# Kernel tuning notes

Measured on AMD Instinct MI355X. Metric: run time of the kernel, lower is better.

The kernel has to match this reference:

```python
import jax, jax.numpy as jnp
import numpy as np
from jax import lax

B, N, D_MODEL = 2, 1024, 512
D_INNER, D_STATE, D_CONV, DT_RANK, RED = 1024, 16, 4, 32, 4
EPS = 1e-5


def setup_inputs() -> dict:
    key = jax.random.key(0)
    ks = jax.random.split(key, 40)
    f32 = jnp.float32
    inp = {}
    inp["I1"] = jax.random.normal(ks[0], (B, N, D_MODEL), f32)
    inp["I2"] = jax.random.normal(ks[1], (B, N, D_MODEL), f32)
    inp["norm1_w"] = jnp.ones((D_MODEL,), f32)
    inp["norm1_b"] = jnp.zeros((D_MODEL,), f32)
    inp["norm2_w"] = jnp.ones((D_MODEL,), f32)
    inp["norm2_b"] = jnp.zeros((D_MODEL,), f32)
    inp["se_w1"] = jax.random.normal(ks[2], (D_MODEL // RED, D_MODEL), f32) * 0.02
    inp["se_w2"] = jax.random.normal(ks[3], (D_MODEL, D_MODEL // RED), f32) * 0.02
    A = jnp.tile(jnp.arange(1, D_STATE + 1, dtype=f32), (D_INNER, 1))  # (d_inner, d_state)
    for i, base in ((1, 4), (2, 14)):
        p = f"m{i}_"
        inp[p + "in_w"] = jax.random.normal(ks[base + 0], (2 * D_INNER, D_MODEL), f32) * 0.02
        inp[p + "conv_w"] = jax.random.normal(ks[base + 1], (D_INNER, 1, D_CONV), f32) * 0.1
        inp[p + "conv_b"] = jnp.zeros((D_INNER,), f32)
        inp[p + "xproj_w"] = jax.random.normal(ks[base + 2], (DT_RANK + 2 * D_STATE, D_INNER), f32) * 0.02
        inp[p + "dt_w"] = jax.random.normal(ks[base + 3], (D_INNER, DT_RANK), f32) * 0.02
        inp[p + "dt_b"] = jax.random.normal(ks[base + 4], (D_INNER,), f32) * 0.1
        inp[p + "A_log"] = jnp.log(A)
        inp[p + "D"] = jnp.ones((D_INNER,), f32)
        inp[p + "out_w"] = jax.random.normal(ks[base + 5], (D_MODEL, D_INNER), f32) * 0.02
    return inp


def layernorm(x, w, b):
    mu = x.mean(-1, keepdims=True)
    var = ((x - mu) ** 2).mean(-1, keepdims=True)
    return (x - mu) * lax.rsqrt(var + EPS) * w + b


def silu(x):
    return x * jax.nn.sigmoid(x)


def mamba(x, in_w, conv_w, conv_b, xproj_w, dt_w, dt_b, A_log, Dp, out_w):
    # x: (B, L, d_model)
    b, L, _ = x.shape
    xz = x @ in_w.T                        # (B, L, 2*d_inner)
    xc, z = jnp.split(xz, 2, axis=-1)
    # depthwise causal conv1d over L
    xc = xc.transpose(0, 2, 1)             # (B, d_inner, L)
    xc = jnp.pad(xc, ((0, 0), (0, 0), (D_CONV - 1, 0)))
    xc = lax.conv_general_dilated(xc, conv_w, (1,), "VALID",
                                  dimension_numbers=("NCH", "OIH", "NCH"),
                                  feature_group_count=D_INNER)
    xc = silu(xc + conv_b[None, :, None]).transpose(0, 2, 1)  # (B, L, d_inner)
    x_dbl = xc @ xproj_w.T                 # (B, L, dt_rank + 2*d_state)
    dt, Bm, Cm = jnp.split(x_dbl, [DT_RANK, DT_RANK + D_STATE], axis=-1)
    dt = jax.nn.softplus(dt @ dt_w.T + dt_b)      # (B, L, d_inner)
    A = -jnp.exp(A_log)                           # (d_inner, d_state)
    dA = jnp.exp(dt[..., None] * A)               # (B, L, d_inner, d_state)
    dBu = dt[..., None] * Bm[:, :, None, :] * xc[..., None]

    def step(h, inputs):
        dA_t, dBu_t, C_t = inputs
        h = dA_t * h + dBu_t                      # (B, d_inner, d_state)
        y = jnp.einsum("bds,bs->bd", h, C_t)
        return h, y

    h0 = jnp.zeros((b, D_INNER, D_STATE), x.dtype)
    _, ys = lax.scan(step, h0, (dA.transpose(1, 0, 2, 3),
                                dBu.transpose(1, 0, 2, 3),
                                Cm.transpose(1, 0, 2)))
    y = ys.transpose(1, 0, 2)                     # (B, L, d_inner)
    y = y + xc * Dp
    y = y * silu(z)
    return y @ out_w.T                            # (B, L, d_model)


def se_block(x, w1, w2):
    y = x.mean(axis=1)                            # (B, C)
    y = jax.nn.sigmoid(jax.nn.relu(y @ w1.T) @ w2.T)
    return x * y[:, None, :]


def channel_exchange(x1, x2):
    c = x1.shape[-1]
    mask = (jnp.arange(c) % 2 == 0)               # swap channels where c % p == 0
    return jnp.where(mask, x2, x1), jnp.where(mask, x1, x2)


def reference(I1, I2, norm1_w, norm1_b, norm2_w, norm2_b, se_w1, se_w2,
              m1_in_w, m1_conv_w, m1_conv_b, m1_xproj_w, m1_dt_w, m1_dt_b, m1_A_log, m1_D, m1_out_w,
              m2_in_w, m2_conv_w, m2_conv_b, m2_xproj_w, m2_dt_w, m2_dt_b, m2_A_log, m2_D, m2_out_w):
    I1n = layernorm(I1, norm1_w, norm1_b)
    I2n = layernorm(I2, norm2_w, norm2_b)
    s1, s2 = channel_exchange(I1n, I2n)
    s1 = se_block(s1, se_w1, se_w2)
    s2 = se_block(s2, se_w1, se_w2)
    o1 = mamba(s1, m1_in_w, m1_conv_w, m1_conv_b, m1_xproj_w, m1_dt_w, m1_dt_b, m1_A_log, m1_D, m1_out_w) + I1
    o2 = mamba(s2, m2_in_w, m2_conv_w, m2_conv_b, m2_xproj_w, m2_dt_w, m2_dt_b, m2_A_log, m2_D, m2_out_w) + I2
    return (o1, o2)
```

## Files before the change

kernel.cpp:

```cpp
#include <hip/hip_runtime.h>
#include <hip/hip_bf16.h>

constexpr int kB   = 2;
constexpr int kN   = 1024;
constexpr int kDM  = 512;
constexpr int kDI  = 1024;
constexpr int kDS  = 16;
constexpr int kDTR = 32;
constexpr int kNC  = 32;
constexpr int kCL  = 32;

typedef __attribute__((ext_vector_type(8))) __bf16 bf16x8;
typedef __attribute__((ext_vector_type(4))) __bf16 bf16x4;
typedef __attribute__((ext_vector_type(4))) float  f32x4;

__device__ __forceinline__ float sigmoidf_(float x) { return 1.f / (1.f + __expf(-x)); }
__device__ __forceinline__ float sum4(float4 a) { return a.x + a.y + a.z + a.w; }
__device__ __forceinline__ float dot4(float4 a) { return a.x*a.x + a.y*a.y + a.z*a.z + a.w*a.w; }
__device__ __forceinline__ float4 nrm4(float4 x, float mu, float rs, float4 w, float4 b) {
    return make_float4((x.x-mu)*rs*w.x + b.x, (x.y-mu)*rs*w.y + b.y,
                       (x.z-mu)*rs*w.z + b.z, (x.w-mu)*rs*w.w + b.w);
}

__launch_bounds__(256)
__global__ void ln_exchange_k(const float* __restrict__ I1, const float* __restrict__ I2,
                              const float* __restrict__ w1, const float* __restrict__ b1,
                              const float* __restrict__ w2, const float* __restrict__ b2,
                              float* __restrict__ s1, float* __restrict__ s2)
{
    int row  = blockIdx.x * 4 + (threadIdx.x >> 6);
    int lane = threadIdx.x & 63;
    const float4* p1 = reinterpret_cast<const float4*>(I1 + (size_t)row * kDM);
    const float4* p2 = reinterpret_cast<const float4*>(I2 + (size_t)row * kDM);
    float4 xa1 = p1[lane], xb1 = p1[lane + 64];
    float4 xa2 = p2[lane], xb2 = p2[lane + 64];
    float su1 = sum4(xa1) + sum4(xb1), sq1 = dot4(xa1) + dot4(xb1);
    float su2 = sum4(xa2) + sum4(xb2), sq2 = dot4(xa2) + dot4(xb2);
    #pragma unroll
    for (int m = 32; m; m >>= 1) {
        su1 += __shfl_xor(su1, m, 64); sq1 += __shfl_xor(sq1, m, 64);
        su2 += __shfl_xor(su2, m, 64); sq2 += __shfl_xor(sq2, m, 64);
    }
    float mu1 = su1 * (1.f / kDM), v1 = sq1 * (1.f / kDM) - mu1 * mu1;
    float mu2 = su2 * (1.f / kDM), v2 = sq2 * (1.f / kDM) - mu2 * mu2;
    float rs1 = rsqrtf(v1 + 1e-5f), rs2 = rsqrtf(v2 + 1e-5f);
    const float4* W1 = reinterpret_cast<const float4*>(w1);
    const float4* B1 = reinterpret_cast<const float4*>(b1);
    const float4* W2 = reinterpret_cast<const float4*>(w2);
    const float4* B2 = reinterpret_cast<const float4*>(b2);
    float4 w1a = W1[lane], w1b = W1[lane+64], b1a = B1[lane], b1b = B1[lane+64];
    float4 w2a = W2[lane], w2b = W2[lane+64], b2a = B2[lane], b2b = B2[lane+64];
    float4 n1a = nrm4(xa1, mu1, rs1, w1a, b1a), n1b = nrm4(xb1, mu1, rs1, w1b, b1b);
    float4 n2a = nrm4(xa2, mu2, rs2, w2a, b2a), n2b = nrm4(xb2, mu2, rs2, w2b, b2b);
    float4 o1a = make_float4(n2a.x, n1a.y, n2a.z, n1a.w);
    float4 o2a = make_float4(n1a.x, n2a.y, n1a.z, n2a.w);
    float4 o1b = make_float4(n2b.x, n1b.y, n2b.z, n1b.w);
    float4 o2b = make_float4(n1b.x, n2b.y, n1b.z, n2b.w);
    float4* q1 = reinterpret_cast<float4*>(s1 + (size_t)row * kDM);
    float4* q2 = reinterpret_cast<float4*>(s2 + (size_t)row * kDM);
    q1[lane] = o1a; q1[lane + 64] = o1b;
    q2[lane] = o2a; q2[lane + 64] = o2b;
}

__launch_bounds__(256)
__global__ void col_sum_k(const float* __restrict__ s1, const float* __restrict__ s2,
                          float* __restrict__ partial)
{
    int x = blockIdx.x;
    int t  = x & 1;
    int b  = (x >> 1) & 1;
    int cc = (x >> 2) & 1;
    int nc = x >> 3;
    int c = cc * 256 + threadIdx.x;
    const float* src = (t ? s2 : s1) + (size_t)b * kN * kDM + (size_t)nc * 128 * kDM + c;
    float acc = 0.f;
    for (int n = 0; n < 128; ++n) acc += src[(size_t)n * kDM];
    partial[(((size_t)(t * 2 + b)) * 8 + nc) * kDM + c] = acc;
}

__launch_bounds__(128)
__global__ void se_mlp_k(const float* __restrict__ partial,
                         const float* __restrict__ w1, const float* __restrict__ w2,
                         float* __restrict__ scl1, float* __restrict__ scl2)
{
    int t = blockIdx.x >> 1, b = blockIdx.x & 1;
    const float* part = partial + ((size_t)(t * 2 + b)) * 8 * kDM;
    float* scl = (t ? scl2 : scl1) + b * kDM;
    __shared__ float m[kDM];
    __shared__ float hid[128];
    for (int c = threadIdx.x; c < kDM; c += 128) {
        float acc = 0.f;
        #pragma unroll
        for (int nc = 0; nc < 8; ++nc) acc += part[nc * kDM + c];
        m[c] = acc * (1.f / kN);
    }
    __syncthreads();
    int j = threadIdx.x;
    float acc = 0.f;
    for (int c = 0; c < kDM; ++c) acc = fmaf(m[c], w1[j * kDM + c], acc);
    hid[j] = fmaxf(acc, 0.f);
    __syncthreads();
    for (int c = j; c < kDM; c += 128) {
        float a2 = 0.f;
        for (int k = 0; k < 128; ++k) a2 = fmaf(hid[k], w2[c * 128 + k], a2);
        scl[c] = sigmoidf_(a2);
    }
}

__launch_bounds__(256)
__global__ void scale_cvt_k(const float* __restrict__ s1f, const float* __restrict__ s2f,
                            const float* __restrict__ scl1, const float* __restrict__ scl2,
                            __bf16* __restrict__ out1, __bf16* __restrict__ out2)
{
    int gidx = blockIdx.x * 256 + threadIdx.x;
    int mam = gidx >> 18;
    int idx = gidx & 262143;
    const float* s = mam ? s2f : s1f;
    const float* scl = mam ? scl2 : scl1;
    __bf16* out = mam ? out2 : out1;
    float4 v = reinterpret_cast<const float4*>(s)[idx];
    int c4 = idx & 127;
    int row = idx >> 7;
    int b = row >> 10;
    float4 sc = reinterpret_cast<const float4*>(scl + b * kDM)[c4];
    bf16x4 o = { (__bf16)(v.x * sc.x), (__bf16)(v.y * sc.y),
                 (__bf16)(v.z * sc.z), (__bf16)(v.w * sc.w) };
    reinterpret_cast<bf16x4*>(out)[idx] = o;
}

__launch_bounds__(256)
__global__ void cvt_all_k(const float* __restrict__ in0, __bf16* __restrict__ win0,
                          const float* __restrict__ xp0, __bf16* __restrict__ wxp0,
                          const float* __restrict__ ow0, __bf16* __restrict__ wow0,
                          const float* __restrict__ in1, __bf16* __restrict__ win1,
                          const float* __restrict__ xp1, __bf16* __restrict__ wxp1,
                          const float* __restrict__ ow1, __bf16* __restrict__ wow1)
{
    int idx = blockIdx.x * 256 + threadIdx.x;
    const float* src; __bf16* dst; int base;
    if (idx < 262144)      { src = in0; dst = win0; base = 0; }
    else if (idx < 278528) { src = xp0; dst = wxp0; base = 262144; }
    else if (idx < 409600) { src = ow0; dst = wow0; base = 278528; }
    else if (idx < 671744) { src = in1; dst = win1; base = 409600; }
    else if (idx < 688128) { src = xp1; dst = wxp1; base = 671744; }
    else                   { src = ow1; dst = wow1; base = 688128; }
    int i = idx - base;
    float4 v = reinterpret_cast<const float4*>(src)[i];
    bf16x4 o = { (__bf16)v.x, (__bf16)v.y, (__bf16)v.z, (__bf16)v.w };
    reinterpret_cast<bf16x4*>(dst)[i] = o;
}

template<int WM16, int WN16, bool ADD_RES>
__global__ __launch_bounds__(256) void gemm_bt2(
    const __bf16* __restrict__ A0, const __bf16* __restrict__ A1,
    const __bf16* __restrict__ B0, const __bf16* __restrict__ B1,
    const float* __restrict__ R0, const float* __restrict__ R1,
    float* __restrict__ C0, float* __restrict__ C1,
    int M, int N, int K)
{
    constexpr int WM = 16 * WM16, WN = 16 * WN16;
    int tiles_n = N / WN;
    int tiles_m = M / WM;
    int per = tiles_m * tiles_n;
    int wave = blockIdx.x * (blockDim.x >> 6) + (threadIdx.x >> 6);
    int mam = wave >= per;
    if (mam) wave -= per;
    const __bf16* A  = mam ? A1 : A0;
    const __bf16* Bw = mam ? B1 : B0;
    const float*  R  = mam ? R1 : R0;
    float*        C  = mam ? C1 : C0;
    int tm = wave / tiles_n, tn = wave % tiles_n;
    int lane = threadIdx.x & 63;
    int r = lane & 15;
    int ko = (lane >> 4) * 8;
    const __bf16* Abase = A  + (size_t)(tm * WM + r) * K + ko;
    const __bf16* Bbase = Bw + (size_t)(tn * WN + r) * K + ko;
    f32x4 acc[WM16][WN16];
    #pragma unroll
    for (int i = 0; i < WM16; ++i)
        #pragma unroll
        for (int j = 0; j < WN16; ++j)
            acc[i][j] = (f32x4){0.f, 0.f, 0.f, 0.f};
    for (int k0 = 0; k0 < K; k0 += 32) {
        bf16x8 a[WM16], b[WN16];
        #pragma unroll
        for (int i = 0; i < WM16; ++i)
            a[i] = *reinterpret_cast<const bf16x8*>(Abase + (size_t)i * 16 * K + k0);
        #pragma unroll
        for (int j = 0; j < WN16; ++j)
            b[j] = *reinterpret_cast<const bf16x8*>(Bbase + (size_t)j * 16 * K + k0);
        #pragma unroll
        for (int i = 0; i < WM16; ++i)
            #pragma unroll
            for (int j = 0; j < WN16; ++j)
                acc[i][j] = __builtin_amdgcn_mfma_f32_16x16x32_bf16(a[i], b[j], acc[i][j], 0, 0, 0);
    }
    int row0 = tm * WM + ((lane >> 4) << 2);
    int col0 = tn * WN + (lane & 15);
    #pragma unroll
    for (int i = 0; i < WM16; ++i)
        #pragma unroll
        for (int j = 0; j < WN16; ++j)
            #pragma unroll
            for (int rr = 0; rr < 4; ++rr) {
                size_t idx = (size_t)(row0 + i * 16 + rr) * N + col0 + j * 16;
                float v = acc[i][j][rr];
                if (ADD_RES) v += R[idx];
                C[idx] = v;
            }
}

__launch_bounds__(256)
__global__ void conv_silu_k(const float* __restrict__ xz0, const float* __restrict__ xz1,
                            const float* __restrict__ cw0, const float* __restrict__ cw1,
                            const float* __restrict__ cb0, const float* __restrict__ cb1,
                            float* __restrict__ xcf0, float* __restrict__ xcf1,
                            __bf16* __restrict__ xcb0, __bf16* __restrict__ xcb1)
{
    int gidx = blockIdx.x * 256 + threadIdx.x;
    int mam = gidx >> 21;
    int idx = gidx & ((1 << 21) - 1);
    const float* xz = mam ? xz1 : xz0;
    const float* cw = mam ? cw1 : cw0;
    const float* cb = mam ? cb1 : cb0;
    float* xcf = mam ? xcf1 : xcf0;
    __bf16* xcb = mam ? xcb1 : xcb0;
    int d = idx & (kDI - 1);
    int n = (idx >> 10) & (kN - 1);
    int b = idx >> 20;
    const float* base = xz + (size_t)(b << 10) * (2 * kDI) + d;
    float acc = cb[d];
    #pragma unroll
    for (int j = 0; j < 4; ++j) {
        int nn = n - 3 + j;
        if (nn >= 0) acc = fmaf(base[(size_t)nn * (2 * kDI)], cw[d * 4 + j], acc);
    }
    float o = acc * sigmoidf_(acc);
    xcf[idx] = o;
    xcb[idx] = (__bf16)o;
}

__launch_bounds__(256)
__global__ void dt_softplus_k(const float* __restrict__ xd0, const float* __restrict__ xd1,
                              const float* __restrict__ dtw0, const float* __restrict__ dtw1,
                              const float* __restrict__ dtb0, const float* __restrict__ dtb1,
                              float* __restrict__ out0, float* __restrict__ out1)
{
    int idx = blockIdx.x * 256 + threadIdx.x;
    int d = idx & (kDI - 1);
    int rest = idx >> 10;
    int mblk = rest & 511;
    int mam = rest >> 9;
    const float* xd  = mam ? xd1 : xd0;
    const float* dtw = mam ? dtw1 : dtw0;
    float bias = (mam ? dtb1 : dtb0)[d];
    float* dtout = mam ? out1 : out0;
    float w[kDTR];
    const float4* wv = reinterpret_cast<const float4*>(dtw + (size_t)d * kDTR);
    #pragma unroll
    for (int q = 0; q < 8; ++q) {
        float4 v = wv[q];
        w[q*4+0] = v.x; w[q*4+1] = v.y; w[q*4+2] = v.z; w[q*4+3] = v.w;
    }
    #pragma unroll
    for (int mi = 0; mi < 4; ++mi) {
        int m = mblk * 4 + mi;
        const float4* xv = reinterpret_cast<const float4*>(xd + (size_t)m * 64);
        float acc = bias;
        #pragma unroll
        for (int q = 0; q < 8; ++q) {
            float4 v = xv[q];
            acc = fmaf(v.x, w[q*4+0], acc);
            acc = fmaf(v.y, w[q*4+1], acc);
            acc = fmaf(v.z, w[q*4+2], acc);
            acc = fmaf(v.w, w[q*4+3], acc);
        }
        float sp = acc > 15.f ? acc : log1pf(__expf(acc));
        dtout[(size_t)m * kDI + d] = sp;
    }
}

__device__ __forceinline__ size_t ph_idx(int bm, int c, int s, int d) {
    return (((size_t)bm * kNC + c) * kDS + s) * kDI + d;
}

__launch_bounds__(256)
__global__ void scan_p1(const float* __restrict__ dt_0, const float* __restrict__ dt_1,
                        const float* __restrict__ xc_0, const float* __restrict__ xc_1,
                        const float* __restrict__ xd_0, const float* __restrict__ xd_1,
                        const float* __restrict__ Al_0, const float* __restrict__ Al_1,
                        float* __restrict__ Pbuf, float* __restrict__ Hbuf)
{
    int bid = blockIdx.x;
    int dgrp = bid & 3;
    int c    = (bid >> 2) & (kNC - 1);
    int b    = (bid >> 7) & 1;
    int mam  = bid >> 8;
    int d    = dgrp * 256 + threadIdx.x;
    int bm   = mam * 2 + b;
    const float* dtp = mam ? dt_1 : dt_0;
    const float* xcp = mam ? xc_1 : xc_0;
    const float* xdp = mam ? xd_1 : xd_0;
    const float* Alp = mam ? Al_1 : Al_0;

    float a[kDS], h[kDS], P[kDS];
    {
        const float4* Av = reinterpret_cast<const float4*>(Alp + d * kDS);
        #pragma unroll
        for (int q = 0; q < 4; ++q) {
            float4 v = Av[q];
            a[q*4+0] = -__expf(v.x); a[q*4+1] = -__expf(v.y);
            a[q*4+2] = -__expf(v.z); a[q*4+3] = -__expf(v.w);
        }
    }
    #pragma unroll
    for (int s = 0; s < kDS; ++s) { h[s] = 0.f; P[s] = 1.f; }

    int t0 = c * kCL;
    const float* dtr = dtp + ((size_t)b * kN + t0) * kDI + d;
    const float* xcr = xcp + ((size_t)b * kN + t0) * kDI + d;
    const float4* xdr = reinterpret_cast<const float4*>(xdp + ((size_t)b * kN + t0) * 64);

    #pragma unroll 4
    for (int t = 0; t < kCL; ++t) {
        float dtv = dtr[(size_t)t * kDI];
        float xcv = xcr[(size_t)t * kDI];
        float4 B0 = xdr[t * 16 + 8],  B1 = xdr[t * 16 + 9];
        float4 B2 = xdr[t * 16 + 10], B3 = xdr[t * 16 + 11];
        float Bv[kDS] = {B0.x,B0.y,B0.z,B0.w, B1.x,B1.y,B1.z,B1.w,
                         B2.x,B2.y,B2.z,B2.w, B3.x,B3.y,B3.z,B3.w};
        float dtxc = dtv * xcv;
        #pragma unroll
        for (int s = 0; s < kDS; ++s) {
            float dA = __expf(dtv * a[s]);
            P[s] *= dA;
            h[s] = fmaf(dA, h[s], dtxc * Bv[s]);
        }
    }
    #pragma unroll
    for (int s = 0; s < kDS; ++s) {
        Pbuf[ph_idx(bm, c, s, d)] = P[s];
        Hbuf[ph_idx(bm, c, s, d)] = h[s];
    }
}

__launch_bounds__(256)
__global__ void scan_p2(const float* __restrict__ Pbuf, const float* __restrict__ Hbuf,
                        float* __restrict__ Init)
{
    int i = blockIdx.x * 256 + threadIdx.x;
    int d = i & (kDI - 1);
    int s = (i >> 10) & 15;
    int bm = i >> 14;
    float h = 0.f;
    #pragma unroll 4
    for (int c = 0; c < kNC; ++c) {
        size_t o = ph_idx(bm, c, s, d);
        Init[o] = h;
        h = fmaf(Pbuf[o], h, Hbuf[o]);
    }
}

__launch_bounds__(256)
__global__ void scan_p3(const float* __restrict__ dt_0, const float* __restrict__ dt_1,
                        const float* __restrict__ xc_0, const float* __restrict__ xc_1,
                        const float* __restrict__ xz_0, const float* __restrict__ xz_1,
                        const float* __restrict__ xd_0, const float* __restrict__ xd_1,
                        const float* __restrict__ Al_0, const float* __restrict__ Al_1,
                        const float* __restrict__ Dp_0, const float* __restrict__ Dp_1,
                        const float* __restrict__ Init,
                        __bf16* __restrict__ yg_0, __bf16* __restrict__ yg_1)
{
    int bid = blockIdx.x;
    int dgrp = bid & 3;
    int c    = (bid >> 2) & (kNC - 1);
    int b    = (bid >> 7) & 1;
    int mam  = bid >> 8;
    int d    = dgrp * 256 + threadIdx.x;
    int bm   = mam * 2 + b;
    const float* dtp = mam ? dt_1 : dt_0;
    const float* xcp = mam ? xc_1 : xc_0;
    const float* xzp = mam ? xz_1 : xz_0;
    const float* xdp = mam ? xd_1 : xd_0;
    const float* Alp = mam ? Al_1 : Al_0;
    const float* Dpp = mam ? Dp_1 : Dp_0;
    __bf16* ygp = mam ? yg_1 : yg_0;

    float a[kDS], h[kDS];
    {
        const float4* Av = reinterpret_cast<const float4*>(Alp + d * kDS);
        #pragma unroll
        for (int q = 0; q < 4; ++q) {
            float4 v = Av[q];
            a[q*4+0] = -__expf(v.x); a[q*4+1] = -__expf(v.y);
            a[q*4+2] = -__expf(v.z); a[q*4+3] = -__expf(v.w);
        }
    }
    #pragma unroll
    for (int s = 0; s < kDS; ++s) h[s] = Init[ph_idx(bm, c, s, d)];
    float Dd = Dpp[d];

    int t0 = c * kCL;
    const float* dtr = dtp + ((size_t)b * kN + t0) * kDI + d;
    const float* xcr = xcp + ((size_t)b * kN + t0) * kDI + d;
    const float* zr  = xzp + ((size_t)b * kN + t0) * 2 * kDI + kDI + d;
    const float4* xdr = reinterpret_cast<const float4*>(xdp + ((size_t)b * kN + t0) * 64);
    __bf16* yr = ygp + ((size_t)b * kN + t0) * kDI + d;

    #pragma unroll 4
    for (int t = 0; t < kCL; ++t) {
        float dtv = dtr[(size_t)t * kDI];
        float xcv = xcr[(size_t)t * kDI];
        float zv  = zr[(size_t)t * 2 * kDI];
        float4 B0 = xdr[t * 16 + 8],  B1 = xdr[t * 16 + 9];
        float4 B2 = xdr[t * 16 + 10], B3 = xdr[t * 16 + 11];
        float4 C0 = xdr[t * 16 + 12], C1 = xdr[t * 16 + 13];
        float4 C2 = xdr[t * 16 + 14], C3 = xdr[t * 16 + 15];
        float Bv[kDS] = {B0.x,B0.y,B0.z,B0.w, B1.x,B1.y,B1.z,B1.w,
                         B2.x,B2.y,B2.z,B2.w, B3.x,B3.y,B3.z,B3.w};
        float Cv[kDS] = {C0.x,C0.y,C0.z,C0.w, C1.x,C1.y,C1.z,C1.w,
                         C2.x,C2.y,C2.z,C2.w, C3.x,C3.y,C3.z,C3.w};
        float dtxc = dtv * xcv;
        float acc0 = 0.f, acc1 = 0.f, acc2 = 0.f, acc3 = 0.f;
        #pragma unroll
        for (int s = 0; s < kDS; s += 4) {
            float dA0 = __expf(dtv * a[s+0]);
            float dA1 = __expf(dtv * a[s+1]);
            float dA2 = __expf(dtv * a[s+2]);
            float dA3 = __expf(dtv * a[s+3]);
            h[s+0] = fmaf(dA0, h[s+0], dtxc * Bv[s+0]);
            h[s+1] = fmaf(dA1, h[s+1], dtxc * Bv[s+1]);
            h[s+2] = fmaf(dA2, h[s+2], dtxc * Bv[s+2]);
            h[s+3] = fmaf(dA3, h[s+3], dtxc * Bv[s+3]);
            acc0 = fmaf(h[s+0], Cv[s+0], acc0);
            acc1 = fmaf(h[s+1], Cv[s+1], acc1);
            acc2 = fmaf(h[s+2], Cv[s+2], acc2);
            acc3 = fmaf(h[s+3], Cv[s+3], acc3);
        }
        float y = (acc0 + acc1) + (acc2 + acc3) + xcv * Dd;
        yr[(size_t)t * kDI] = (__bf16)(y * zv * sigmoidf_(zv));
    }
}

extern "C" void kernel_launch(void* const* d_in, const int* in_sizes, int n_in,
                              void* d_out, int out_size, void* d_ws, size_t ws_size,
                              hipStream_t stream)
{
    (void)in_sizes; (void)n_in; (void)out_size; (void)ws_size;
    const float* I1  = (const float*)d_in[0];
    const float* I2  = (const float*)d_in[1];
    const float* n1w = (const float*)d_in[2];
    const float* n1b = (const float*)d_in[3];
    const float* n2w = (const float*)d_in[4];
    const float* n2b = (const float*)d_in[5];
    const float* sew1 = (const float*)d_in[6];
    const float* sew2 = (const float*)d_in[7];
    const float* in_w[2]   = {(const float*)d_in[8],  (const float*)d_in[17]};
    const float* conv_w[2] = {(const float*)d_in[9],  (const float*)d_in[18]};
    const float* conv_b[2] = {(const float*)d_in[10], (const float*)d_in[19]};
    const float* xp_w[2]   = {(const float*)d_in[11], (const float*)d_in[20]};
    const float* dt_w[2]   = {(const float*)d_in[12], (const float*)d_in[21]};
    const float* dt_b[2]   = {(const float*)d_in[13], (const float*)d_in[22]};
    const float* A_log[2]  = {(const float*)d_in[14], (const float*)d_in[23]};
    const float* Dp[2]     = {(const float*)d_in[15], (const float*)d_in[24]};
    const float* out_w[2]  = {(const float*)d_in[16], (const float*)d_in[25]};

    char* base = (char*)d_ws;
    size_t off = 0;
    auto alloc = [&](size_t bytes) -> char* {
        char* p = base + off;
        off = (off + bytes + 255) & ~(size_t)255;
        return p;
    };
    float*   s1   = (float*)alloc((size_t)4 << 20);
    float*   s2   = (float*)alloc((size_t)4 << 20);
    float*   partial = (float*)alloc(2 * 2 * 8 * kDM * 4);
    float*   scl1 = (float*)alloc(1024 * 4);
    float*   scl2 = (float*)alloc(1024 * 4);
    __bf16*  sA[2]    = {(__bf16*)alloc((size_t)2 << 20), (__bf16*)alloc((size_t)2 << 20)};
    __bf16*  w_in[2]  = {(__bf16*)alloc((size_t)2 << 20), (__bf16*)alloc((size_t)2 << 20)};
    __bf16*  w_xp[2]  = {(__bf16*)alloc((size_t)128 << 10), (__bf16*)alloc((size_t)128 << 10)};
    __bf16*  w_out[2] = {(__bf16*)alloc((size_t)1 << 20), (__bf16*)alloc((size_t)1 << 20)};
    float*   xz[2]  = {(float*)alloc((size_t)16 << 20), (float*)alloc((size_t)16 << 20)};
    float*   xcf[2] = {(float*)alloc((size_t)8 << 20),  (float*)alloc((size_t)8 << 20)};
    __bf16*  xcb[2] = {(__bf16*)alloc((size_t)4 << 20), (__bf16*)alloc((size_t)4 << 20)};
    float*   xd[2]  = {(float*)alloc((size_t)512 << 10), (float*)alloc((size_t)512 << 10)};
    float*   dts[2] = {(float*)alloc((size_t)8 << 20),  (float*)alloc((size_t)8 << 20)};
    __bf16*  yg[2]  = {(__bf16*)alloc((size_t)4 << 20), (__bf16*)alloc((size_t)4 << 20)};
    float*   Hbuf   = (float*)alloc((size_t)8 << 20);
    float*   Init   = (float*)alloc((size_t)8 << 20);
    float*   Pbuf   = s1;
    float* o1 = (float*)d_out;
    float* o2 = o1 + (size_t)kB * kN * kDM;

    ln_exchange_k<<<512, 256, 0, stream>>>(I1, I2, n1w, n1b, n2w, n2b, s1, s2);
    col_sum_k<<<64, 256, 0, stream>>>(s1, s2, partial);
    se_mlp_k<<<4, 128, 0, stream>>>(partial, sew1, sew2, scl1, scl2);
    scale_cvt_k<<<2048, 256, 0, stream>>>(s1, s2, scl1, scl2, sA[0], sA[1]);
    cvt_all_k<<<3200, 256, 0, stream>>>(in_w[0], w_in[0], xp_w[0], w_xp[0], out_w[0], w_out[0],
                                        in_w[1], w_in[1], xp_w[1], w_xp[1], out_w[1], w_out[1]);
    gemm_bt2<4, 8, false><<<256, 256, 0, stream>>>(sA[0], sA[1], w_in[0], w_in[1],
                                                   nullptr, nullptr, xz[0], xz[1],
                                                   kB * kN, 2 * kDI, kDM);
    conv_silu_k<<<16384, 256, 0, stream>>>(xz[0], xz[1], conv_w[0], conv_w[1],
                                           conv_b[0], conv_b[1], xcf[0], xcf[1],
                                           xcb[0], xcb[1]);
    gemm_bt2<1, 1, false><<<256, 256, 0, stream>>>(xcb[0], xcb[1], w_xp[0], w_xp[1],
                                                   nullptr, nullptr, xd[0], xd[1],
                                                   kB * kN, 64, kDI);
    dt_softplus_k<<<4096, 256, 0, stream>>>(xd[0], xd[1], dt_w[0], dt_w[1],
                                            dt_b[0], dt_b[1], dts[0], dts[1]);
    scan_p1<<<512, 256, 0, stream>>>(dts[0], dts[1], xcf[0], xcf[1], xd[0], xd[1],
                                     A_log[0], A_log[1], Pbuf, Hbuf);
    scan_p2<<<256, 256, 0, stream>>>(Pbuf, Hbuf, Init);
    scan_p3<<<512, 256, 0, stream>>>(dts[0], dts[1], xcf[0], xcf[1], xz[0], xz[1],
                                     xd[0], xd[1], A_log[0], A_log[1], Dp[0], Dp[1],
                                     Init, yg[0], yg[1]);
    gemm_bt2<2, 4, true><<<256, 256, 0, stream>>>(yg[0], yg[1], w_out[0], w_out[1],
                                                  I1, I2, o1, o2, kB * kN, kDM, kDI);
}
```

Measured before the change: 222.3 us.

## Store intermediates in bf16, fuse column sums into layernorm, merge conversion kernels

The layernorm/exchange kernel now writes bf16 activations and per-block column partial sums directly, which removes the separate column-sum kernel and its fp32 reread. The SE scale and weight-conversion kernels are merged into one launch. The in-projection GEMM writes xz in bf16, the conv no longer writes an fp32 copy, and the scans read bf16 x and z, roughly halving traffic on the large intermediates. The x-proj GEMM tile shape changes and the SE MLP reduces over 256 partials per batch. Storing these intermediates in bf16 adds rounding on values that were fp32 before.

```diff
diff --git a/kernel.cpp b/kernel.cpp
--- a/kernel.cpp
+++ b/kernel.cpp
@@ -21,14 +21,19 @@
     return make_float4((x.x-mu)*rs*w.x + b.x, (x.y-mu)*rs*w.y + b.y,
                        (x.z-mu)*rs*w.z + b.z, (x.w-mu)*rs*w.w + b.w);
 }
+__device__ __forceinline__ bf16x4 tob4(float4 v) {
+    return (bf16x4){(__bf16)v.x, (__bf16)v.y, (__bf16)v.z, (__bf16)v.w};
+}
 
 __launch_bounds__(256)
 __global__ void ln_exchange_k(const float* __restrict__ I1, const float* __restrict__ I2,
                               const float* __restrict__ w1, const float* __restrict__ b1,
                               const float* __restrict__ w2, const float* __restrict__ b2,
-                              float* __restrict__ s1, float* __restrict__ s2)
-{
-    int row  = blockIdx.x * 4 + (threadIdx.x >> 6);
+                              __bf16* __restrict__ s1b, __bf16* __restrict__ s2b,
+                              float* __restrict__ partial)
+{
+    int w    = threadIdx.x >> 6;
+    int row  = blockIdx.x * 4 + w;
     int lane = threadIdx.x & 63;
     const float4* p1 = reinterpret_cast<const float4*>(I1 + (size_t)row * kDM);
     const float4* p2 = reinterpret_cast<const float4*>(I2 + (size_t)row * kDM);
@@ -56,51 +61,50 @@
     float4 o2a = make_float4(n1a.x, n2a.y, n1a.z, n2a.w);
     float4 o1b = make_float4(n2b.x, n1b.y, n2b.z, n1b.w);
     float4 o2b = make_float4(n1b.x, n2b.y, n1b.z, n2b.w);
-    float4* q1 = reinterpret_cast<float4*>(s1 + (size_t)row * kDM);
-    float4* q2 = reinterpret_cast<float4*>(s2 + (size_t)row * kDM);
-    q1[lane] = o1a; q1[lane + 64] = o1b;
-    q2[lane] = o2a; q2[lane + 64] = o2b;
-}
-
-__launch_bounds__(256)
-__global__ void col_sum_k(const float* __restrict__ s1, const float* __restrict__ s2,
-                          float* __restrict__ partial)
-{
-    int x = blockIdx.x;
-    int t  = x & 1;
-    int b  = (x >> 1) & 1;
-    int cc = (x >> 2) & 1;
-    int nc = x >> 3;
-    int c = cc * 256 + threadIdx.x;
-    const float* src = (t ? s2 : s1) + (size_t)b * kN * kDM + (size_t)nc * 128 * kDM + c;
-    float acc = 0.f;
-    for (int n = 0; n < 128; ++n) acc += src[(size_t)n * kDM];
-    partial[(((size_t)(t * 2 + b)) * 8 + nc) * kDM + c] = acc;
-}
-
-__launch_bounds__(128)
+    bf16x4* q1 = reinterpret_cast<bf16x4*>(s1b + (size_t)row * kDM);
+    bf16x4* q2 = reinterpret_cast<bf16x4*>(s2b + (size_t)row * kDM);
+    q1[lane] = tob4(o1a); q1[lane + 64] = tob4(o1b);
+    q2[lane] = tob4(o2a); q2[lane + 64] = tob4(o2b);
+
+    __shared__ float lp[2][4][kDM];
+    int c0 = lane * 4, c1 = 256 + lane * 4;
+    lp[0][w][c0+0] = o1a.x; lp[0][w][c0+1] = o1a.y; lp[0][w][c0+2] = o1a.z; lp[0][w][c0+3] = o1a.w;
+    lp[0][w][c1+0] = o1b.x; lp[0][w][c1+1] = o1b.y; lp[0][w][c1+2] = o1b.z; lp[0][w][c1+3] = o1b.w;
+    lp[1][w][c0+0] = o2a.x; lp[1][w][c0+1] = o2a.y; lp[1][w][c0+2] = o2a.z; lp[1][w][c0+3] = o2a.w;
+    lp[1][w][c1+0] = o2b.x; lp[1][w][c1+1] = o2b.y; lp[1][w][c1+2] = o2b.z; lp[1][w][c1+3] = o2b.w;
+    __syncthreads();
+    for (int c = threadIdx.x; c < kDM; c += 256) {
+        partial[((size_t)0 * 512 + blockIdx.x) * kDM + c] =
+            lp[0][0][c] + lp[0][1][c] + lp[0][2][c] + lp[0][3][c];
+        partial[((size_t)1 * 512 + blockIdx.x) * kDM + c] =
+            lp[1][0][c] + lp[1][1][c] + lp[1][2][c] + lp[1][3][c];
+    }
+}
+
+__launch_bounds__(256)
 __global__ void se_mlp_k(const float* __restrict__ partial,
                          const float* __restrict__ w1, const float* __restrict__ w2,
                          float* __restrict__ scl1, float* __restrict__ scl2)
 {
     int t = blockIdx.x >> 1, b = blockIdx.x & 1;
-    const float* part = partial + ((size_t)(t * 2 + b)) * 8 * kDM;
     float* scl = (t ? scl2 : scl1) + b * kDM;
     __shared__ float m[kDM];
     __shared__ float hid[128];
-    for (int c = threadIdx.x; c < kDM; c += 128) {
+    const float* pb = partial + ((size_t)t * 512 + b * 256) * kDM;
+    for (int c = threadIdx.x; c < kDM; c += 256) {
         float acc = 0.f;
-        #pragma unroll
-        for (int nc = 0; nc < 8; ++nc) acc += part[nc * kDM + c];
+        for (int k = 0; k < 256; ++k) acc += pb[(size_t)k * kDM + c];
         m[c] = acc * (1.f / kN);
     }
     __syncthreads();
-    int j = threadIdx.x;
-    float acc = 0.f;
-    for (int c = 0; c < kDM; ++c) acc = fmaf(m[c], w1[j * kDM + c], acc);
-    hid[j] = fmaxf(acc, 0.f);
+    if (threadIdx.x < 128) {
+        int j = threadIdx.x;
+        float acc = 0.f;
+        for (int c = 0; c < kDM; ++c) acc = fmaf(m[c], w1[j * kDM + c], acc);
+        hid[j] = fmaxf(acc, 0.f);
+    }
     __syncthreads();
-    for (int c = j; c < kDM; c += 128) {
+    for (int c = threadIdx.x; c < kDM; c += 256) {
         float a2 = 0.f;
         for (int k = 0; k < 128; ++k) a2 = fmaf(hid[k], w2[c * 128 + k], a2);
         scl[c] = sigmoidf_(a2);
@@ -108,35 +112,38 @@
 }
 
 __launch_bounds__(256)
-__global__ void scale_cvt_k(const float* __restrict__ s1f, const float* __restrict__ s2f,
-                            const float* __restrict__ scl1, const float* __restrict__ scl2,
-                            __bf16* __restrict__ out1, __bf16* __restrict__ out2)
+__global__ void scale_cvt_all_k(const __bf16* __restrict__ s1b, const __bf16* __restrict__ s2b,
+                                const float* __restrict__ scl1, const float* __restrict__ scl2,
+                                __bf16* __restrict__ sA0, __bf16* __restrict__ sA1,
+                                const float* __restrict__ in0, __bf16* __restrict__ win0,
+                                const float* __restrict__ xp0, __bf16* __restrict__ wxp0,
+                                const float* __restrict__ ow0, __bf16* __restrict__ wow0,
+                                const float* __restrict__ in1, __bf16* __restrict__ win1,
+                                const float* __restrict__ xp1, __bf16* __restrict__ wxp1,
+                                const float* __restrict__ ow1, __bf16* __restrict__ wow1)
 {
     int gidx = blockIdx.x * 256 + threadIdx.x;
-    int mam = gidx >> 18;
-    int idx = gidx & 262143;
-    const float* s = mam ? s2f : s1f;
-    const float* scl = mam ? scl2 : scl1;
-    __bf16* out = mam ? out2 : out1;
-    float4 v = reinterpret_cast<const float4*>(s)[idx];
-    int c4 = idx & 127;
-    int row = idx >> 7;
-    int b = row >> 10;
-    float4 sc = reinterpret_cast<const float4*>(scl + b * kDM)[c4];
-    bf16x4 o = { (__bf16)(v.x * sc.x), (__bf16)(v.y * sc.y),
-                 (__bf16)(v.z * sc.z), (__bf16)(v.w * sc.w) };
-    reinterpret_cast<bf16x4*>(out)[idx] = o;
-}
-
-__launch_bounds__(256)
-__global__ void cvt_all_k(const float* __restrict__ in0, __bf16* __restrict__ win0,
-                          const float* __restrict__ xp0, __bf16* __restrict__ wxp0,
-                          const float* __restrict__ ow0, __bf16* __restrict__ wow0,
-                          const float* __restrict__ in1, __bf16* __restrict__ win1,
-                          const float* __restrict__ xp1, __bf16* __restrict__ wxp1,
-                          const float* __restrict__ ow1, __bf16* __restrict__ wow1)
-{
-    int idx = blockIdx.x * 256 + threadIdx.x;
+    if (gidx < 262144) {
+        int mam = gidx >> 17;
+        int i = gidx & 131071;
+        const __bf16* s = mam ? s2b : s1b;
+        const float* scl = mam ? scl2 : scl1;
+        __bf16* out = mam ? sA1 : sA0;
+        bf16x8 v = reinterpret_cast<const bf16x8*>(s)[i];
+        int cg = (i & 63) * 2;
+        int row = i >> 6;
+        int b = row >> 10;
+        const float4* sp = reinterpret_cast<const float4*>(scl + b * kDM);
+        float4 sa = sp[cg], sb = sp[cg + 1];
+        bf16x8 o;
+        o[0] = (__bf16)((float)v[0] * sa.x); o[1] = (__bf16)((float)v[1] * sa.y);
+        o[2] = (__bf16)((float)v[2] * sa.z); o[3] = (__bf16)((float)v[3] * sa.w);
+        o[4] = (__bf16)((float)v[4] * sb.x); o[5] = (__bf16)((float)v[5] * sb.y);
+        o[6] = (__bf16)((float)v[6] * sb.z); o[7] = (__bf16)((float)v[7] * sb.w);
+        reinterpret_cast<bf16x8*>(out)[i] = o;
+        return;
+    }
+    int idx = gidx - 262144;
     const float* src; __bf16* dst; int base;
     if (idx < 262144)      { src = in0; dst = win0; base = 0; }
     else if (idx < 278528) { src = xp0; dst = wxp0; base = 262144; }
@@ -146,16 +153,15 @@
     else                   { src = ow1; dst = wow1; base = 688128; }
     int i = idx - base;
     float4 v = reinterpret_cast<const float4*>(src)[i];
-    bf16x4 o = { (__bf16)v.x, (__bf16)v.y, (__bf16)v.z, (__bf16)v.w };
-    reinterpret_cast<bf16x4*>(dst)[i] = o;
-}
-
-template<int WM16, int WN16, bool ADD_RES>
+    reinterpret_cast<bf16x4*>(dst)[i] = tob4(v);
+}
+
+template<int WM16, int WN16, bool ADD_RES, typename OT>
 __global__ __launch_bounds__(256) void gemm_bt2(
     const __bf16* __restrict__ A0, const __bf16* __restrict__ A1,
     const __bf16* __restrict__ B0, const __bf16* __restrict__ B1,
     const float* __restrict__ R0, const float* __restrict__ R1,
-    float* __restrict__ C0, float* __restrict__ C1,
+    OT* __restrict__ C0, OT* __restrict__ C1,
     int M, int N, int K)
 {
     constexpr int WM = 16 * WM16, WN = 16 * WN16;
@@ -168,7 +174,7 @@
     const __bf16* A  = mam ? A1 : A0;
     const __bf16* Bw = mam ? B1 : B0;
     const float*  R  = mam ? R1 : R0;
-    float*        C  = mam ? C1 : C0;
+    OT*           C  = mam ? C1 : C0;
     int tm = wave / tiles_n, tn = wave % tiles_n;
     int lane = threadIdx.x & 63;
     int r = lane & 15;
@@ -206,37 +212,34 @@
                 size_t idx = (size_t)(row0 + i * 16 + rr) * N + col0 + j * 16;
                 float v = acc[i][j][rr];
                 if (ADD_RES) v += R[idx];
-                C[idx] = v;
+                C[idx] = (OT)v;
             }
 }
 
 __launch_bounds__(256)
-__global__ void conv_silu_k(const float* __restrict__ xz0, const float* __restrict__ xz1,
+__global__ void conv_silu_k(const __bf16* __restrict__ xz0, const __bf16* __restrict__ xz1,
                             const float* __restrict__ cw0, const float* __restrict__ cw1,
                             const float* __restrict__ cb0, const float* __restrict__ cb1,
-                            float* __restrict__ xcf0, float* __restrict__ xcf1,
                             __bf16* __restrict__ xcb0, __bf16* __restrict__ xcb1)
 {
     int gidx = blockIdx.x * 256 + threadIdx.x;
     int mam = gidx >> 21;
     int idx = gidx & ((1 << 21) - 1);
-    const float* xz = mam ? xz1 : xz0;
+    const __bf16* xz = mam ? xz1 : xz0;
     const float* cw = mam ? cw1 : cw0;
     const float* cb = mam ? cb1 : cb0;
-    float* xcf = mam ? xcf1 : xcf0;
     __bf16* xcb = mam ? xcb1 : xcb0;
     int d = idx & (kDI - 1);
     int n = (idx >> 10) & (kN - 1);
     int b = idx >> 20;
-    const float* base = xz + (size_t)(b << 10) * (2 * kDI) + d;
+    const __bf16* base = xz + (size_t)(b << 10) * (2 * kDI) + d;
     float acc = cb[d];
     #pragma unroll
     for (int j = 0; j < 4; ++j) {
         int nn = n - 3 + j;
-        if (nn >= 0) acc = fmaf(base[(size_t)nn * (2 * kDI)], cw[d * 4 + j], acc);
+        if (nn >= 0) acc = fmaf((float)base[(size_t)nn * (2 * kDI)], cw[d * 4 + j], acc);
     }
     float o = acc * sigmoidf_(acc);
-    xcf[idx] = o;
     xcb[idx] = (__bf16)o;
 }
 
@@ -286,7 +289,7 @@
 
 __launch_bounds__(256)
 __global__ void scan_p1(const float* __restrict__ dt_0, const float* __restrict__ dt_1,
-                        const float* __restrict__ xc_0, const float* __restrict__ xc_1,
+                        const __bf16* __restrict__ xc_0, const __bf16* __restrict__ xc_1,
                         const float* __restrict__ xd_0, const float* __restrict__ xd_1,
                         const float* __restrict__ Al_0, const float* __restrict__ Al_1,
                         float* __restrict__ Pbuf, float* __restrict__ Hbuf)
@@ -299,7 +302,7 @@
     int d    = dgrp * 256 + threadIdx.x;
     int bm   = mam * 2 + b;
     const float* dtp = mam ? dt_1 : dt_0;
-    const float* xcp = mam ? xc_1 : xc_0;
+    const __bf16* xcp = mam ? xc_1 : xc_0;
     const float* xdp = mam ? xd_1 : xd_0;
     const float* Alp = mam ? Al_1 : Al_0;
 
@@ -318,13 +321,13 @@
 
     int t0 = c * kCL;
     const float* dtr = dtp + ((size_t)b * kN + t0) * kDI + d;
-    const float* xcr = xcp + ((size_t)b * kN + t0) * kDI + d;
+    const __bf16* xcr = xcp + ((size_t)b * kN + t0) * kDI + d;
     const float4* xdr = reinterpret_cast<const float4*>(xdp + ((size_t)b * kN + t0) * 64);
 
     #pragma unroll 4
     for (int t = 0; t < kCL; ++t) {
         float dtv = dtr[(size_t)t * kDI];
-        float xcv = xcr[(size_t)t * kDI];
+        float xcv = (float)xcr[(size_t)t * kDI];
         float4 B0 = xdr[t * 16 + 8],  B1 = xdr[t * 16 + 9];
         float4 B2 = xdr[t * 16 + 10], B3 = xdr[t * 16 + 11];
         float Bv[kDS] = {B0.x,B0.y,B0.z,B0.w, B1.x,B1.y,B1.z,B1.w,
@@ -363,8 +366,8 @@
 
 __launch_bounds__(256)
 __global__ void scan_p3(const float* __restrict__ dt_0, const float* __restrict__ dt_1,
-                        const float* __restrict__ xc_0, const float* __restrict__ xc_1,
-                        const float* __restrict__ xz_0, const float* __restrict__ xz_1,
+                        const __bf16* __restrict__ xc_0, const __bf16* __restrict__ xc_1,
+                        const __bf16* __restrict__ xz_0, const __bf16* __restrict__ xz_1,
                         const float* __restrict__ xd_0, const float* __restrict__ xd_1,
                         const float* __restrict__ Al_0, const float* __restrict__ Al_1,
                         const float* __restrict__ Dp_0, const float* __restrict__ Dp_1,
@@ -379,8 +382,8 @@
     int d    = dgrp * 256 + threadIdx.x;
     int bm   = mam * 2 + b;
     const float* dtp = mam ? dt_1 : dt_0;
-    const float* xcp = mam ? xc_1 : xc_0;
-    const float* xzp = mam ? xz_1 : xz_0;
+    const __bf16* xcp = mam ? xc_1 : xc_0;
+    const __bf16* xzp = mam ? xz_1 : xz_0;
     const float* xdp = mam ? xd_1 : xd_0;
     const float* Alp = mam ? Al_1 : Al_0;
     const float* Dpp = mam ? Dp_1 : Dp_0;
@@ -402,16 +405,16 @@
 
     int t0 = c * kCL;
     const float* dtr = dtp + ((size_t)b * kN + t0) * kDI + d;
-    const float* xcr = xcp + ((size_t)b * kN + t0) * kDI + d;
-    const float* zr  = xzp + ((size_t)b * kN + t0) * 2 * kDI + kDI + d;
+    const __bf16* xcr = xcp + ((size_t)b * kN + t0) * kDI + d;
+    const __bf16* zr  = xzp + ((size_t)b * kN + t0) * 2 * kDI + kDI + d;
     const float4* xdr = reinterpret_cast<const float4*>(xdp + ((size_t)b * kN + t0) * 64);
     __bf16* yr = ygp + ((size_t)b * kN + t0) * kDI + d;
 
     #pragma unroll 4
     for (int t = 0; t < kCL; ++t) {
         float dtv = dtr[(size_t)t * kDI];
-        float xcv = xcr[(size_t)t * kDI];
-        float zv  = zr[(size_t)t * 2 * kDI];
+        float xcv = (float)xcr[(size_t)t * kDI];
+        float zv  = (float)zr[(size_t)t * 2 * kDI];
         float4 B0 = xdr[t * 16 + 8],  B1 = xdr[t * 16 + 9];
         float4 B2 = xdr[t * 16 + 10], B3 = xdr[t * 16 + 11];
         float4 C0 = xdr[t * 16 + 12], C1 = xdr[t * 16 + 13];
@@ -472,50 +475,49 @@
         off = (off + bytes + 255) & ~(size_t)255;
         return p;
     };
-    float*   s1   = (float*)alloc((size_t)4 << 20);
-    float*   s2   = (float*)alloc((size_t)4 << 20);
-    float*   partial = (float*)alloc(2 * 2 * 8 * kDM * 4);
+    __bf16*  s1b  = (__bf16*)alloc((size_t)2 << 20);
+    __bf16*  s2b  = (__bf16*)alloc((size_t)2 << 20);
+    float*   partial = (float*)alloc((size_t)2 * 512 * kDM * 4);
     float*   scl1 = (float*)alloc(1024 * 4);
     float*   scl2 = (float*)alloc(1024 * 4);
     __bf16*  sA[2]    = {(__bf16*)alloc((size_t)2 << 20), (__bf16*)alloc((size_t)2 << 20)};
     __bf16*  w_in[2]  = {(__bf16*)alloc((size_t)2 << 20), (__bf16*)alloc((size_t)2 << 20)};
     __bf16*  w_xp[2]  = {(__bf16*)alloc((size_t)128 << 10), (__bf16*)alloc((size_t)128 << 10)};
     __bf16*  w_out[2] = {(__bf16*)alloc((size_t)1 << 20), (__bf16*)alloc((size_t)1 << 20)};
-    float*   xz[2]  = {(float*)alloc((size_t)16 << 20), (float*)alloc((size_t)16 << 20)};
-    float*   xcf[2] = {(float*)alloc((size_t)8 << 20),  (float*)alloc((size_t)8 << 20)};
+    __bf16*  xzb[2] = {(__bf16*)alloc((size_t)8 << 20), (__bf16*)alloc((size_t)8 << 20)};
     __bf16*  xcb[2] = {(__bf16*)alloc((size_t)4 << 20), (__bf16*)alloc((size_t)4 << 20)};
     float*   xd[2]  = {(float*)alloc((size_t)512 << 10), (float*)alloc((size_t)512 << 10)};
     float*   dts[2] = {(float*)alloc((size_t)8 << 20),  (float*)alloc((size_t)8 << 20)};
     __bf16*  yg[2]  = {(__bf16*)alloc((size_t)4 << 20), (__bf16*)alloc((size_t)4 << 20)};
+    float*   Pbuf   = (float*)alloc((size_t)8 << 20);
     float*   Hbuf   = (float*)alloc((size_t)8 << 20);
     float*   Init   = (float*)alloc((size_t)8 << 20);
-    float*   Pbuf   = s1;
     float* o1 = (float*)d_out;
     float* o2 = o1 + (size_t)kB * kN * kDM;
 
-    ln_exchange_k<<<512, 256, 0, stream>>>(I1, I2, n1w, n1b, n2w, n2b, s1, s2);
-    col_sum_k<<<64, 256, 0, stream>>>(s1, s2, partial);
-    se_mlp_k<<<4, 128, 0, stream>>>(partial, sew1, sew2, scl1, scl2);
-    scale_cvt_k<<<2048, 256, 0, stream>>>(s1, s2, scl1, scl2, sA[0], sA[1]);
-    cvt_all_k<<<3200, 256, 0, stream>>>(in_w[0], w_in[0], xp_w[0], w_xp[0], out_w[0], w_out[0],
-                                        in_w[1], w_in[1], xp_w[1], w_xp[1], out_w[1], w_out[1]);
-    gemm_bt2<4, 8, false><<<256, 256, 0, stream>>>(sA[0], sA[1], w_in[0], w_in[1],
-                                                   nullptr, nullptr, xz[0], xz[1],
-                                                   kB * kN, 2 * kDI, kDM);
-    conv_silu_k<<<16384, 256, 0, stream>>>(xz[0], xz[1], conv_w[0], conv_w[1],
-                                           conv_b[0], conv_b[1], xcf[0], xcf[1],
-                                           xcb[0], xcb[1]);
-    gemm_bt2<1, 1, false><<<256, 256, 0, stream>>>(xcb[0], xcb[1], w_xp[0], w_xp[1],
-                                                   nullptr, nullptr, xd[0], xd[1],
-                                                   kB * kN, 64, kDI);
+    ln_exchange_k<<<512, 256, 0, stream>>>(I1, I2, n1w, n1b, n2w, n2b, s1b, s2b, partial);
+    se_mlp_k<<<4, 256, 0, stream>>>(partial, sew1, sew2, scl1, scl2);
+    scale_cvt_all_k<<<4224, 256, 0, stream>>>(s1b, s2b, scl1, scl2, sA[0], sA[1],
+                                              in_w[0], w_in[0], xp_w[0], w_xp[0],
+                                              out_w[0], w_out[0],
+                                              in_w[1], w_in[1], xp_w[1], w_xp[1],
+                                              out_w[1], w_out[1]);
+    gemm_bt2<4, 8, false, __bf16><<<256, 256, 0, stream>>>(
+        sA[0], sA[1], w_in[0], w_in[1], nullptr, nullptr, xzb[0], xzb[1],
+        kB * kN, 2 * kDI, kDM);
+    conv_silu_k<<<16384, 256, 0, stream>>>(xzb[0], xzb[1], conv_w[0], conv_w[1],
+                                           conv_b[0], conv_b[1], xcb[0], xcb[1]);
+    gemm_bt2<1, 2, false, float><<<128, 256, 0, stream>>>(
+        xcb[0], xcb[1], w_xp[0], w_xp[1], nullptr, nullptr, xd[0], xd[1],
+        kB * kN, 64, kDI);
     dt_softplus_k<<<4096, 256, 0, stream>>>(xd[0], xd[1], dt_w[0], dt_w[1],
                                             dt_b[0], dt_b[1], dts[0], dts[1]);
-    scan_p1<<<512, 256, 0, stream>>>(dts[0], dts[1], xcf[0], xcf[1], xd[0], xd[1],
+    scan_p1<<<512, 256, 0, stream>>>(dts[0], dts[1], xcb[0], xcb[1], xd[0], xd[1],
                                      A_log[0], A_log[1], Pbuf, Hbuf);
     scan_p2<<<256, 256, 0, stream>>>(Pbuf, Hbuf, Init);
-    scan_p3<<<512, 256, 0, stream>>>(dts[0], dts[1], xcf[0], xcf[1], xz[0], xz[1],
+    scan_p3<<<512, 256, 0, stream>>>(dts[0], dts[1], xcb[0], xcb[1], xzb[0], xzb[1],
                                      xd[0], xd[1], A_log[0], A_log[1], Dp[0], Dp[1],
                                      Init, yg[0], yg[1]);
-    gemm_bt2<2, 4, true><<<256, 256, 0, stream>>>(yg[0], yg[1], w_out[0], w_out[1],
-                                                  I1, I2, o1, o2, kB * kN, kDM, kDI);
-}
+    gemm_bt2<2, 4, true, float><<<256, 256, 0, stream>>>(
+        yg[0], yg[1], w_out[0], w_out[1], I1, I2, o1, o2, kB * kN, kDM, kDI);
+}
```

Result: slower. 232.0 us (+4.4%).
